# Kernel tuning notes

Hardware: AMD Instinct MI355X
Metric: run time of the kernel (lower is better)

The kernel has to match this reference:

```python
import jax, jax.numpy as jnp
import numpy as np

# hp / hp_mask constants
B = 1024          # batch_size
S = 4096          # seq_length (raw timesteps)
PATCH = 8         # patch_size
P = S // PATCH    # num patches = 512 (second dim of x)
K = 128           # dimension
P_M, P_R, P_E = 0.8, 0.1, 0.1
CORR = 0.15       # Corruption_ratio
NUM_MASK = int(B * P_M)
NUM_RAND = int(B * P_R)
MAX_CORR = int(CORR * S / PATCH)  # max corrupted patches per row = 76


def setup_inputs() -> dict:
    key = jax.random.key(0)
    k1, k2, k3, k4 = jax.random.split(key, 4)
    x = jax.random.normal(k1, (B, P, K), dtype=jnp.float32)
    pos = jax.random.normal(k2, (P, K), dtype=jnp.float32)
    w_mask = jax.random.normal(k3, (K,), dtype=jnp.float32)  # nn.Linear(1,K,bias=False) weight col
    seq_len = jax.random.randint(k4, (B,), PATCH, S + 1)     # per-sample raw length
    return {"x": x, "pos": pos, "w_mask": w_mask, "seq_len": seq_len}


def reference(x, pos, w_mask, seq_len):
    key = jax.random.key(42)
    kp, ks, kr = jax.random.split(key, 3)

    # --- batch-level mask_type assignment (permute batch, split into 3 groups) ---
    perm = jax.random.permutation(kp, B)
    mask_type = jnp.zeros((B,), dtype=jnp.float32)
    mask_type = mask_type.at[perm[:NUM_MASK]].set(0.0)
    mask_type = mask_type.at[perm[NUM_MASK:NUM_MASK + NUM_RAND]].set(1.0)
    mask_type = mask_type.at[perm[NUM_MASK + NUM_RAND:]].set(2.0)

    # --- per-row sampling without replacement over valid patches ---
    n_valid = (seq_len // PATCH).astype(jnp.int32)                                   # [B]
    n_corr = jnp.floor(CORR * seq_len.astype(jnp.float32) / PATCH).astype(jnp.int32)  # [B]
    scores = jax.random.uniform(ks, (B, P))
    valid = jnp.arange(P)[None, :] < n_valid[:, None]
    scores = jnp.where(valid, scores, jnp.inf)
    order = jnp.argsort(scores, axis=1)   # [B,P] patch ids, random order among valid first
    rank = jnp.argsort(order, axis=1)     # rank of each patch position
    sel = rank < n_corr[:, None]          # [B,P] bool: patch selected for corruption

    # padded index output (replaces ragged list I; -1 = pad)
    slot_valid = jnp.arange(MAX_CORR)[None, :] < n_corr[:, None]
    I = jnp.where(slot_valid, order[:, :MAX_CORR], -1)

    # --- replacement values (branch on mask_type[0], as in the original code) ---
    mask_vec = w_mask                                        # Linear(1,K)(1.0)
    rand_vals = jax.random.uniform(kr, (B, P, K))
    repl_mask = mask_vec[None, None, :] + pos[None, :, :]    # [1,P,K] -> broadcast
    repl_rand = rand_vals + pos[None, :, :]                  # [B,P,K]
    t0 = mask_type[0]
    repl = jnp.where(t0 == 0.0, repl_mask, jnp.where(t0 == 1.0, repl_rand, x))
    x_out = jnp.where(sel[:, :, None], repl, x)
    return x_out, I, mask_type
```

## Files before the change

### kernel.cpp

```cpp
#include <hip/hip_runtime.h>
#include <cstdint>
#include <cstring>

#define JAX_PARTITIONABLE 1

#define B_ 1024
#define P_ 512
#define K_ 128
#define MAXC 76
#define NSCORE 524288ull
#define NRAND  67108864ull
#define OFF_I  ((size_t)B_ * P_ * K_)
#define OFF_MT (OFF_I + (size_t)B_ * MAXC)

__host__ __device__ inline uint32_t rotl32(uint32_t v, int d) {
    return (v << d) | (v >> (32 - d));
}

__host__ __device__ inline void tf2x32(uint32_t k0, uint32_t k1,
                                       uint32_t x0, uint32_t x1,
                                       uint32_t& o0, uint32_t& o1) {
    uint32_t ks2 = k0 ^ k1 ^ 0x1BD11BDAu;
    x0 += k0; x1 += k1;
#define TF_R(r) { x0 += x1; x1 = rotl32(x1, (r)); x1 ^= x0; }
    TF_R(13) TF_R(15) TF_R(26) TF_R(6)
    x0 += k1;  x1 += ks2 + 1u;
    TF_R(17) TF_R(29) TF_R(16) TF_R(24)
    x0 += ks2; x1 += k0 + 2u;
    TF_R(13) TF_R(15) TF_R(26) TF_R(6)
    x0 += k0;  x1 += k1 + 3u;
    TF_R(17) TF_R(29) TF_R(16) TF_R(24)
    x0 += k1;  x1 += ks2 + 4u;
    TF_R(13) TF_R(15) TF_R(26) TF_R(6)
    x0 += ks2; x1 += k0 + 5u;
#undef TF_R
    o0 = x0; o1 = x1;
}

__host__ __device__ inline uint32_t jax_bits(uint32_t k0, uint32_t k1,
                                             uint64_t i, uint64_t n) {
#if JAX_PARTITIONABLE
    (void)n;
    uint32_t o0, o1;
    tf2x32(k0, k1, (uint32_t)(i >> 32), (uint32_t)i, o0, o1);
    return o0 ^ o1;
#else
    uint64_t half = n >> 1;
    uint32_t o0, o1;
    if (i < half) { tf2x32(k0, k1, (uint32_t)i, (uint32_t)(i + half), o0, o1); return o0; }
    tf2x32(k0, k1, (uint32_t)(i - half), (uint32_t)i, o0, o1); return o1;
#endif
}

__device__ inline float u01(uint32_t bits) {
    return __uint_as_float((bits >> 9) | 0x3F800000u) - 1.0f;
}

__global__ void __launch_bounds__(64) mt_kernel(float* __restrict__ mt_out,
                                                uint32_t s0, uint32_t s1) {
    __shared__ uint32_t keys[B_];
    int tid = threadIdx.x;
    for (int j = tid; j < B_; j += 64)
        keys[j] = jax_bits(s0, s1, (uint64_t)j, (uint64_t)B_);
    __syncthreads();
    int i = blockIdx.x * 64 + tid;
    uint32_t ki = keys[i];
    int rank = 0;
    for (int q = 0; q < B_; q++) {
        uint32_t kq = keys[q];
        rank += (kq < ki) || (kq == ki && q < i);
    }
    mt_out[i] = rank < 819 ? 0.0f : (rank < 921 ? 1.0f : 2.0f);
}

__global__ void __launch_bounds__(256) sel_kernel(const int* __restrict__ seq_len,
                                                  float* __restrict__ I_out,
                                                  uint32_t ks0, uint32_t ks1) {
    int b = blockIdx.x;
    int tid = threadIdx.x;
    __shared__ float sc[P_];
    int sl = seq_len[b];
    int n_valid = sl >> 3;
    int n_corr = (int)floorf(0.15f * (float)sl / 8.0f);
    for (int p = tid; p < P_; p += 256) {
        float s = __builtin_inff();
        if (p < n_valid) {
            uint32_t bits = jax_bits(ks0, ks1, (uint64_t)b * P_ + p, NSCORE);
            s = u01(bits);
        }
        sc[p] = s;
    }
    if (tid < MAXC && tid >= n_corr) I_out[(size_t)b * MAXC + tid] = -1.0f;
    __syncthreads();
    for (int p = tid; p < P_; p += 256) {
        if (p >= n_valid) continue;
        float sp = sc[p];
        int rank = 0;
        for (int q = 0; q < n_valid; q++) {
            float sq = sc[q];
            rank += (sq < sp) || (sq == sp && q < p);
        }
        if (rank < n_corr) I_out[(size_t)b * MAXC + rank] = (float)p;
    }
}

__global__ void __launch_bounds__(256) xout_kernel(const float* __restrict__ x,
                                                    const float* __restrict__ pos,
                                                    const float* __restrict__ wm,
                                                    const float* __restrict__ I_in,
                                                    float* __restrict__ out,
                                                    int t0, uint32_t kr0, uint32_t kr1) {
    int b = blockIdx.x;
    int tid = threadIdx.x;
    __shared__ uint32_t selmask[P_ / 32];
    if (tid < P_ / 32) selmask[tid] = 0u;
    __syncthreads();
    if (tid < MAXC) {
        float v = I_in[(size_t)b * MAXC + tid];
        if (v >= 0.0f) {
            int p = (int)v;
            atomicOr(&selmask[p >> 5], 1u << (p & 31));
        }
    }
    __syncthreads();

    const float4* x4  = (const float4*)x + (size_t)b * (P_ * (K_ / 4));
    float4*       o4  = (float4*)out     + (size_t)b * (P_ * (K_ / 4));
    const float4* p4  = (const float4*)pos;
    const float4* wm4 = (const float4*)wm;

    for (int i = tid; i < P_ * (K_ / 4); i += 256) {
        int p  = i >> 5;
        int kq = i & 31;
        bool sel = (selmask[p >> 5] >> (p & 31)) & 1u;
        float4 v;
        if (!sel || t0 == 2) {
            v = x4[i];
        } else if (t0 == 0) {
            float4 a = wm4[kq];
            float4 c = p4[p * (K_ / 4) + kq];
            v.x = a.x + c.x; v.y = a.y + c.y; v.z = a.z + c.z; v.w = a.w + c.w;
        } else {
            float4 c = p4[p * (K_ / 4) + kq];
            uint64_t e = (((uint64_t)b * P_ + p) * K_) + (uint64_t)kq * 4;
            v.x = u01(jax_bits(kr0, kr1, e + 0, NRAND)) + c.x;
            v.y = u01(jax_bits(kr0, kr1, e + 1, NRAND)) + c.y;
            v.z = u01(jax_bits(kr0, kr1, e + 2, NRAND)) + c.z;
            v.w = u01(jax_bits(kr0, kr1, e + 3, NRAND)) + c.w;
        }
        o4[i] = v;
    }
}

extern "C" void kernel_launch(void* const* d_in, const int* in_sizes, int n_in,
                              void* d_out, int out_size, void* d_ws, size_t ws_size,
                              hipStream_t stream) {
    (void)in_sizes; (void)n_in; (void)d_ws; (void)ws_size; (void)out_size;
    const float* x   = (const float*)d_in[0];
    const float* pos = (const float*)d_in[1];
    const float* wm  = (const float*)d_in[2];
    const int* seq_len = (const int*)d_in[3];
    float* out = (float*)d_out;

    uint32_t kp0, kp1, ks0, ks1, kr0, kr1, sub0, sub1;
#if JAX_PARTITIONABLE
    tf2x32(0u, 42u, 0u, 0u, kp0, kp1);
    tf2x32(0u, 42u, 0u, 1u, ks0, ks1);
    tf2x32(0u, 42u, 0u, 2u, kr0, kr1);
    tf2x32(kp0, kp1, 0u, 1u, sub0, sub1);
#else
    {
        uint32_t a0, b0, a1, b1, a2, b2;
        tf2x32(0u, 42u, 0u, 3u, a0, b0);
        tf2x32(0u, 42u, 1u, 4u, a1, b1);
        tf2x32(0u, 42u, 2u, 5u, a2, b2);
        kp0 = a0; kp1 = a1; ks0 = a2; ks1 = b0; kr0 = b1; kr1 = b2;
        uint32_t c0, d0, c1, d1;
        tf2x32(kp0, kp1, 0u, 2u, c0, d0);
        tf2x32(kp0, kp1, 1u, 3u, c1, d1);
        sub0 = d0; sub1 = d1;
    }
#endif

    static uint32_t skeys[B_];
    for (int i = 0; i < B_; i++) skeys[i] = jax_bits(sub0, sub1, (uint64_t)i, (uint64_t)B_);
    int rank0 = 0;
    for (int q = 1; q < B_; q++) if (skeys[q] < skeys[0]) rank0++;
    int t0 = rank0 < 819 ? 0 : (rank0 < 921 ? 1 : 2);

    float* I_out  = out + OFF_I;
    float* mt_out = out + OFF_MT;

    hipLaunchKernelGGL(mt_kernel, dim3(B_ / 64), dim3(64), 0, stream, mt_out, sub0, sub1);
    hipLaunchKernelGGL(sel_kernel, dim3(B_), dim3(256), 0, stream, seq_len, I_out, ks0, ks1);
    hipLaunchKernelGGL(xout_kernel, dim3(B_), dim3(256), 0, stream,
                       x, pos, wm, I_out, out, t0, kr0, kr1);
}
```

Measured before the change: 508.2 us.

## Fuse patch selection into output kernel and use nontemporal loads/stores

Merges the per-row selection kernel with the output-writing kernel, so the selection bitmask is built directly in shared memory instead of being written to and reread from I_out. It also switches the bulk x copy to nontemporal loads and stores via ext_vector_type, and widens the mt_kernel block from 64 to 256 threads. This removes one kernel launch and a dependent global round trip. In exchange, the memory-bound streaming phase in each block now waits behind the O(n^2) rank computation.

```diff
diff --git a/kernel.cpp b/kernel.cpp
--- a/kernel.cpp
+++ b/kernel.cpp
@@ -12,6 +12,8 @@
 #define NRAND  67108864ull
 #define OFF_I  ((size_t)B_ * P_ * K_)
 #define OFF_MT (OFF_I + (size_t)B_ * MAXC)
+
+typedef float f4 __attribute__((ext_vector_type(4)));
 
 __host__ __device__ inline uint32_t rotl32(uint32_t v, int d) {
     return (v << d) | (v >> (32 - d));
@@ -56,14 +58,14 @@
     return __uint_as_float((bits >> 9) | 0x3F800000u) - 1.0f;
 }
 
-__global__ void __launch_bounds__(64) mt_kernel(float* __restrict__ mt_out,
-                                                uint32_t s0, uint32_t s1) {
+__global__ void __launch_bounds__(256) mt_kernel(float* __restrict__ mt_out,
+                                                 uint32_t s0, uint32_t s1) {
     __shared__ uint32_t keys[B_];
     int tid = threadIdx.x;
-    for (int j = tid; j < B_; j += 64)
+    for (int j = tid; j < B_; j += 256)
         keys[j] = jax_bits(s0, s1, (uint64_t)j, (uint64_t)B_);
     __syncthreads();
-    int i = blockIdx.x * 64 + tid;
+    int i = blockIdx.x * 256 + tid;
     uint32_t ki = keys[i];
     int rank = 0;
     for (int q = 0; q < B_; q++) {
@@ -73,15 +75,25 @@
     mt_out[i] = rank < 819 ? 0.0f : (rank < 921 ? 1.0f : 2.0f);
 }
 
-__global__ void __launch_bounds__(256) sel_kernel(const int* __restrict__ seq_len,
-                                                  float* __restrict__ I_out,
-                                                  uint32_t ks0, uint32_t ks1) {
+__global__ void __launch_bounds__(256) fused_kernel(const float* __restrict__ x,
+                                                    const float* __restrict__ pos,
+                                                    const float* __restrict__ wm,
+                                                    const int* __restrict__ seq_len,
+                                                    float* __restrict__ out,
+                                                    float* __restrict__ I_out,
+                                                    int t0,
+                                                    uint32_t ks0, uint32_t ks1,
+                                                    uint32_t kr0, uint32_t kr1) {
     int b = blockIdx.x;
     int tid = threadIdx.x;
     __shared__ float sc[P_];
+    __shared__ uint32_t selmask[P_ / 32];
+
     int sl = seq_len[b];
     int n_valid = sl >> 3;
     int n_corr = (int)floorf(0.15f * (float)sl / 8.0f);
+
+    if (tid < P_ / 32) selmask[tid] = 0u;
     for (int p = tid; p < P_; p += 256) {
         float s = __builtin_inff();
         if (p < n_valid) {
@@ -92,63 +104,46 @@
     }
     if (tid < MAXC && tid >= n_corr) I_out[(size_t)b * MAXC + tid] = -1.0f;
     __syncthreads();
-    for (int p = tid; p < P_; p += 256) {
-        if (p >= n_valid) continue;
+
+    for (int p = tid; p < n_valid; p += 256) {
         float sp = sc[p];
         int rank = 0;
         for (int q = 0; q < n_valid; q++) {
             float sq = sc[q];
             rank += (sq < sp) || (sq == sp && q < p);
         }
-        if (rank < n_corr) I_out[(size_t)b * MAXC + rank] = (float)p;
-    }
-}
-
-__global__ void __launch_bounds__(256) xout_kernel(const float* __restrict__ x,
-                                                    const float* __restrict__ pos,
-                                                    const float* __restrict__ wm,
-                                                    const float* __restrict__ I_in,
-                                                    float* __restrict__ out,
-                                                    int t0, uint32_t kr0, uint32_t kr1) {
-    int b = blockIdx.x;
-    int tid = threadIdx.x;
-    __shared__ uint32_t selmask[P_ / 32];
-    if (tid < P_ / 32) selmask[tid] = 0u;
-    __syncthreads();
-    if (tid < MAXC) {
-        float v = I_in[(size_t)b * MAXC + tid];
-        if (v >= 0.0f) {
-            int p = (int)v;
+        if (rank < n_corr) {
+            I_out[(size_t)b * MAXC + rank] = (float)p;
             atomicOr(&selmask[p >> 5], 1u << (p & 31));
         }
     }
     __syncthreads();
 
-    const float4* x4  = (const float4*)x + (size_t)b * (P_ * (K_ / 4));
-    float4*       o4  = (float4*)out     + (size_t)b * (P_ * (K_ / 4));
-    const float4* p4  = (const float4*)pos;
-    const float4* wm4 = (const float4*)wm;
+    const f4* x4  = (const f4*)x + (size_t)b * (P_ * (K_ / 4));
+    f4*       o4  = (f4*)out     + (size_t)b * (P_ * (K_ / 4));
+    const f4* p4  = (const f4*)pos;
+    const f4* wm4 = (const f4*)wm;
 
     for (int i = tid; i < P_ * (K_ / 4); i += 256) {
         int p  = i >> 5;
         int kq = i & 31;
         bool sel = (selmask[p >> 5] >> (p & 31)) & 1u;
-        float4 v;
+        f4 v;
         if (!sel || t0 == 2) {
-            v = x4[i];
+            v = __builtin_nontemporal_load(&x4[i]);
         } else if (t0 == 0) {
-            float4 a = wm4[kq];
-            float4 c = p4[p * (K_ / 4) + kq];
-            v.x = a.x + c.x; v.y = a.y + c.y; v.z = a.z + c.z; v.w = a.w + c.w;
+            f4 a = wm4[kq];
+            f4 c = p4[p * (K_ / 4) + kq];
+            v = a + c;
         } else {
-            float4 c = p4[p * (K_ / 4) + kq];
+            f4 c = p4[p * (K_ / 4) + kq];
             uint64_t e = (((uint64_t)b * P_ + p) * K_) + (uint64_t)kq * 4;
             v.x = u01(jax_bits(kr0, kr1, e + 0, NRAND)) + c.x;
             v.y = u01(jax_bits(kr0, kr1, e + 1, NRAND)) + c.y;
             v.z = u01(jax_bits(kr0, kr1, e + 2, NRAND)) + c.z;
             v.w = u01(jax_bits(kr0, kr1, e + 3, NRAND)) + c.w;
         }
-        o4[i] = v;
+        __builtin_nontemporal_store(v, &o4[i]);
     }
 }
 
@@ -191,8 +186,7 @@
     float* I_out  = out + OFF_I;
     float* mt_out = out + OFF_MT;
 
-    hipLaunchKernelGGL(mt_kernel, dim3(B_ / 64), dim3(64), 0, stream, mt_out, sub0, sub1);
-    hipLaunchKernelGGL(sel_kernel, dim3(B_), dim3(256), 0, stream, seq_len, I_out, ks0, ks1);
-    hipLaunchKernelGGL(xout_kernel, dim3(B_), dim3(256), 0, stream,
-                       x, pos, wm, I_out, out, t0, kr0, kr1);
+    hipLaunchKernelGGL(mt_kernel, dim3(B_ / 256), dim3(256), 0, stream, mt_out, sub0, sub1);
+    hipLaunchKernelGGL(fused_kernel, dim3(B_), dim3(256), 0, stream,
+                       x, pos, wm, seq_len, out, I_out, t0, ks0, ks1, kr0, kr1);
 }
```

Result: faster. 477.5 us (-6.0%).
